# Optimization experiments

Hardware: AMD Instinct MI355X
Metric: run time of the kernel (lower is better)

The kernel has to match this reference:

```python
import jax, jax.numpy as jnp
import numpy as np
import math

N_HEADS = 8
D_EMBED = 512
D_CROSS = 768
FF_DIM = 2048
D_HEAD = D_EMBED // N_HEADS


def _gelu_tanh(x):
    # matches the module's hand-written tanh GELU
    return 0.5 * x * (1.0 + jnp.tanh(jnp.sqrt(2.0 / jnp.pi) * (x + 0.044715 * x ** 3)))


def _layer_norm(x, g, b, eps=1e-5):
    mu = jnp.mean(x, axis=-1, keepdims=True)
    var = jnp.var(x, axis=-1, keepdims=True)
    return (x - mu) * jax.lax.rsqrt(var + eps) * g + b


def setup_inputs() -> dict:
    key = jax.random.key(0)
    ks = jax.random.split(key, 20)
    s = 0.02
    inp = {
        "x": jax.random.normal(ks[0], (2, 4096, D_EMBED), jnp.float32),
        "y": jax.random.normal(ks[1], (2, 77, D_CROSS), jnp.float32),
        # self-attention: fused in_proj [D, 3D]
        "sa_in_w": jax.random.normal(ks[2], (D_EMBED, 3 * D_EMBED), jnp.float32) * s,
        "sa_in_b": jnp.zeros((3 * D_EMBED,), jnp.float32),
        "sa_out_w": jax.random.normal(ks[3], (D_EMBED, D_EMBED), jnp.float32) * s,
        "sa_out_b": jnp.zeros((D_EMBED,), jnp.float32),
        # cross-attention
        "ca_q_w": jax.random.normal(ks[4], (D_EMBED, D_EMBED), jnp.float32) * s,
        "ca_q_b": jnp.zeros((D_EMBED,), jnp.float32),
        "ca_k_w": jax.random.normal(ks[5], (D_CROSS, D_EMBED), jnp.float32) * s,
        "ca_k_b": jnp.zeros((D_EMBED,), jnp.float32),
        "ca_v_w": jax.random.normal(ks[6], (D_CROSS, D_EMBED), jnp.float32) * s,
        "ca_v_b": jnp.zeros((D_EMBED,), jnp.float32),
        "ca_out_w": jax.random.normal(ks[7], (D_EMBED, D_EMBED), jnp.float32) * s,
        "ca_out_b": jnp.zeros((D_EMBED,), jnp.float32),
        # feed-forward
        "ff_w1": jax.random.normal(ks[8], (D_EMBED, FF_DIM), jnp.float32) * s,
        "ff_b1": jnp.zeros((FF_DIM,), jnp.float32),
        "ff_w2": jax.random.normal(ks[9], (FF_DIM, D_EMBED), jnp.float32) * s,
        "ff_b2": jnp.zeros((D_EMBED,), jnp.float32),
        # layer norms
        "ln1_g": jnp.ones((D_EMBED,), jnp.float32),
        "ln1_b": jnp.zeros((D_EMBED,), jnp.float32),
        "ln2_g": jnp.ones((D_EMBED,), jnp.float32),
        "ln2_b": jnp.zeros((D_EMBED,), jnp.float32),
        "ln3_g": jnp.ones((D_EMBED,), jnp.float32),
        "ln3_b": jnp.zeros((D_EMBED,), jnp.float32),
    }
    return inp


def _mha(q, k, v):
    # q,k,v: [B, S, D] -> split heads -> attention -> merge
    B, Sq, D = q.shape
    Skv = k.shape[1]
    qh = q.reshape(B, Sq, N_HEADS, D_HEAD).transpose(0, 2, 1, 3)
    kh = k.reshape(B, Skv, N_HEADS, D_HEAD).transpose(0, 2, 1, 3)
    vh = v.reshape(B, Skv, N_HEADS, D_HEAD).transpose(0, 2, 1, 3)
    scores = jnp.einsum("bhqd,bhkd->bhqk", qh, kh) / math.sqrt(D_HEAD)
    w = jax.nn.softmax(scores, axis=-1)
    out = jnp.einsum("bhqk,bhkd->bhqd", w, vh)
    return out.transpose(0, 2, 1, 3).reshape(B, Sq, D)


def reference(x, y, sa_in_w, sa_in_b, sa_out_w, sa_out_b,
              ca_q_w, ca_q_b, ca_k_w, ca_k_b, ca_v_w, ca_v_b, ca_out_w, ca_out_b,
              ff_w1, ff_b1, ff_w2, ff_b2,
              ln1_g, ln1_b, ln2_g, ln2_b, ln3_g, ln3_b):
    # self-attention (no causal mask; default causal_mask=False)
    qkv = x @ sa_in_w + sa_in_b
    q, k, v = jnp.split(qkv, 3, axis=-1)
    sa = _mha(q, k, v) @ sa_out_w + sa_out_b
    x = _layer_norm(x + sa, ln1_g, ln1_b)

    # cross-attention to y
    qc = x @ ca_q_w + ca_q_b
    kc = y @ ca_k_w + ca_k_b
    vc = y @ ca_v_w + ca_v_b
    ca = _mha(qc, kc, vc) @ ca_out_w + ca_out_b
    x = _layer_norm(x + ca, ln2_g, ln2_b)

    # feed-forward with tanh GELU
    ff = _gelu_tanh(x @ ff_w1 + ff_b1) @ ff_w2 + ff_b2
    x = _layer_norm(x + ff, ln3_g, ln3_b)
    return x
```

## Files before the change

kernel.cpp:

```cpp
#include <hip/hip_runtime.h>
#include <stdint.h>

typedef float floatx4 __attribute__((ext_vector_type(4)));
typedef __bf16 bf16x8 __attribute__((ext_vector_type(8)));
typedef unsigned int uintx4 __attribute__((ext_vector_type(4)));
typedef unsigned short ushort_t;

__device__ __forceinline__ float b2f(ushort_t u) {
  union { unsigned int i; float f; } x; x.i = ((unsigned int)u) << 16; return x.f;
}
__device__ __forceinline__ ushort_t f2b(float f) {
  union { float f; unsigned int i; } x; x.f = f;
  unsigned int i = x.i;
  return (ushort_t)((i + 0x7FFFu + ((i >> 16) & 1u)) >> 16);
}
__device__ __forceinline__ unsigned fbits(float f) {
  union { float f; unsigned u; } x; x.f = f; return x.u;
}
__device__ __forceinline__ unsigned pk_rne(float a, float b) {
#if __has_builtin(__builtin_amdgcn_cvt_pk_bf16_f32)
  return __builtin_bit_cast(unsigned, __builtin_amdgcn_cvt_pk_bf16_f32(a, b));
#else
  return (unsigned)f2b(a) | ((unsigned)f2b(b) << 16);
#endif
}
__device__ __forceinline__ unsigned pk_fast(float a, float b) {
#if __has_builtin(__builtin_amdgcn_cvt_pk_bf16_f32)
  return __builtin_bit_cast(unsigned, __builtin_amdgcn_cvt_pk_bf16_f32(a, b));
#else
  return (fbits(b) & 0xFFFF0000u) | (fbits(a) >> 16);
#endif
}
__device__ __forceinline__ uintx4 ld16(const void* p) {
  uintx4 v; __builtin_memcpy(&v, p, 16); return v;
}
__device__ __forceinline__ void st16(void* p, uintx4 v) { __builtin_memcpy(p, &v, 16); }
__device__ __forceinline__ floatx4 f4splat(float x) { floatx4 v = {x, x, x, x}; return v; }
__device__ __forceinline__ void sched_fence() { asm volatile("" ::: "memory"); }

__device__ __forceinline__ floatx4 mfma16(uintx4 a, uintx4 b, floatx4 c) {
  return __builtin_amdgcn_mfma_f32_16x16x32_bf16(
      __builtin_bit_cast(bf16x8, a), __builtin_bit_cast(bf16x8, b), c, 0, 0, 0);
}

__device__ __forceinline__ void gll16(const ushort_t* g, ushort_t* l) {
  __builtin_amdgcn_global_load_lds(
      (__attribute__((address_space(1))) void*)(g),
      (__attribute__((address_space(3))) void*)(l), 16, 0, 0);
}

template <int EPI, int NT>
__global__ __launch_bounds__(256, 2) void gemm_bt(
    const ushort_t* __restrict__ A, const ushort_t* __restrict__ Bt,
    const float* __restrict__ bias, ushort_t* __restrict__ Cout,
    int N, int K) {
  constexpr int NI = NT / 32;
  __shared__ alignas(16) ushort_t lA[128 * 32];
  __shared__ alignas(16) ushort_t lB[NT * 32];
  const int tid = threadIdx.x;
  const int wave = tid >> 6, lane = tid & 63;
  const int quad = lane >> 4, l16 = lane & 15;
  const int bm = blockIdx.y * 128, bn = blockIdx.x * NT;
  const int wm = (wave >> 1) * 64, wn = (wave & 1) * (NT / 2);

  const ushort_t* ag0 = A + (size_t)(bm + wave * 32 + (lane >> 2)) * K + (lane & 3) * 8;
  const ushort_t* ag1 = ag0 + (size_t)16 * K;
  ushort_t* la = lA + wave * 1024;
  const ushort_t* bg0;
  const ushort_t* bg1 = nullptr;
  ushort_t* lb;
  if (NT == 128) {
    bg0 = Bt + (size_t)(bn + wave * 32 + (lane >> 2)) * K + (lane & 3) * 8;
    bg1 = bg0 + (size_t)16 * K;
    lb = lB + wave * 1024;
  } else {
    bg0 = Bt + (size_t)(bn + wave * 16 + (lane >> 2)) * K + (lane & 3) * 8;
    lb = lB + wave * 512;
  }

  floatx4 acc[4][NI];
#pragma unroll
  for (int i = 0; i < 4; i++)
#pragma unroll
    for (int j = 0; j < NI; j++) acc[i][j] = f4splat(0.f);

  for (int k0 = 0; k0 < K; k0 += 32) {
    __syncthreads();
    gll16(ag0 + k0, la);
    gll16(ag1 + k0, la + 512);
    gll16(bg0 + k0, lb);
    if (NT == 128) gll16(bg1 + k0, lb + 512);
    __syncthreads();
    uintx4 af[4], bf[NI];
#pragma unroll
    for (int i = 0; i < 4; i++) af[i] = ld16(&lA[(wm + i * 16 + l16) * 32 + quad * 8]);
#pragma unroll
    for (int i = 0; i < NI; i++) bf[i] = ld16(&lB[(wn + i * 16 + l16) * 32 + quad * 8]);
#pragma unroll
    for (int mi = 0; mi < 4; mi++)
#pragma unroll
      for (int ni = 0; ni < NI; ni++) acc[mi][ni] = mfma16(af[mi], bf[ni], acc[mi][ni]);
  }

  float bv[NI];
#pragma unroll
  for (int ni = 0; ni < NI; ni++) bv[ni] = bias[bn + wn + ni * 16 + l16];

#pragma unroll
  for (int mi = 0; mi < 4; mi++)
#pragma unroll
    for (int ni = 0; ni < NI; ni++)
#pragma unroll
      for (int r = 0; r < 4; r++) {
        int row = bm + wm + mi * 16 + quad * 4 + r;
        int col = bn + wn + ni * 16 + l16;
        float v = acc[mi][ni][r] + bv[ni];
        if (EPI == 2) {
          float w = v + 0.044715f * v * v * v;
          float e = __builtin_amdgcn_exp2f(-2.3022084f * w);
          v = v * __builtin_amdgcn_rcpf(1.f + e);
        }
        Cout[(size_t)row * N + col] = f2b(v);
      }
}

struct TransJob { const float* in; ushort_t* out; int ldi, ldo, nbx, start; };
struct TransJobs6 { TransJob j[6]; };

__global__ __launch_bounds__(256) void prep(TransJobs6 jobs, const float* __restrict__ x,
                                            ushort_t* __restrict__ xbf) {
  __shared__ float t[32][33];
  int bid = blockIdx.x;
  if (bid >= 3584) {
    int i = ((bid - 3584) * 256 + threadIdx.x) * 4;
    float4 v; __builtin_memcpy(&v, x + i, 16);
    unsigned o[2] = {pk_rne(v.x, v.y), pk_rne(v.z, v.w)};
    __builtin_memcpy(xbf + i, o, 8);
    return;
  }
  int ji = 0;
#pragma unroll
  for (int i = 1; i < 6; i++)
    if (bid >= jobs.j[i].start) ji = i;
  TransJob J = jobs.j[ji];
  int local = bid - J.start;
  int by = local / J.nbx, bx = local - by * J.nbx;
  int r0 = by * 32, c0 = bx * 32;
  int tx = threadIdx.x & 31, ty = threadIdx.x >> 5;
#pragma unroll
  for (int i = 0; i < 4; i++)
    t[ty + 8 * i][tx] = J.in[(size_t)(r0 + ty + 8 * i) * J.ldi + c0 + tx];
  __syncthreads();
#pragma unroll
  for (int i = 0; i < 4; i++)
    J.out[(size_t)(c0 + ty + 8 * i) * J.ldo + r0 + tx] = f2b(t[tx][ty + 8 * i]);
}

__global__ __launch_bounds__(256) void mid(
    const ushort_t* __restrict__ qkv, ushort_t* __restrict__ KP,
    ushort_t* __restrict__ VP, const float* __restrict__ y,
    const float* __restrict__ wk, const float* __restrict__ bk,
    const float* __restrict__ wv, const float* __restrict__ bv,
    ushort_t* __restrict__ kc, ushort_t* __restrict__ vc) {
  __shared__ ushort_t t[64 * 72];
  int bid = blockIdx.x;
  int tid = threadIdx.x;
  if (bid < 2048) {
    int g = bid * 256 + tid;
    int lane = g & 63;
    int frag = (g >> 6) & 7;
    int kt = (g >> 9) & 63;
    int bh = g >> 15;
    int b = bh >> 3, h = bh & 7;
    int ni = frag >> 1, kf = frag & 1;
    int l16 = lane & 15, quad = lane >> 4;
    const ushort_t* src = qkv + (size_t)(b * 4096 + kt * 64 + ni * 16 + l16) * 1536 +
                          512 + h * 64 + kf * 32 + quad * 8;
    st16(KP + (size_t)g * 8, ld16(src));
  } else if (bid < 3072) {
    int local = bid - 2048;
    int bh = local >> 6, kt = local & 63;
    int b = bh >> 3, h = bh & 7;
#pragma unroll
    for (int i = 0; i < 2; i++) {
      int c = i * 256 + tid;
      int row = c >> 3, c8 = (c & 7) * 8;
      uintx4 d4 = ld16(qkv + (size_t)(b * 4096 + kt * 64 + row) * 1536 + 1024 + h * 64 + c8);
      ushort_t tmp[8];
      __builtin_memcpy(tmp, &d4, 16);
#pragma unroll
      for (int j = 0; j < 8; j++) t[(c8 + j) * 72 + row] = tmp[j];
    }
    __syncthreads();
#pragma unroll
    for (int i = 0; i < 2; i++) {
      int c = i * 256 + tid;
      int frag = c >> 6, lane = c & 63;
      int f = frag >> 2, dn = frag & 3;
      int l16 = lane & 15, quad = lane >> 4;
      uintx4 d4 = ld16(&t[(dn * 16 + l16) * 72 + f * 32 + quad * 8]);
      st16(VP + ((size_t)(bh * 64 + kt) * 8 + frag) * 512 + (size_t)lane * 8, d4);
    }
  } else {
    int sb = bid - 3072;
    const float* W; const float* B; ushort_t* O;
    if (sb >= 308) { W = wv; B = bv; O = vc; sb -= 308; }
    else           { W = wk; B = bk; O = kc; }
    int idx = sb * 256 + tid;
    if (idx >= 154 * 512) return;
    int r = idx >> 9, col = idx & 511;
    const float* ya = y + (size_t)r * 768;
    float acc = B[col];
#pragma unroll 4
    for (int k = 0; k < 768; k++) acc += ya[k] * W[(size_t)k * 512 + col];
    O[idx] = f2b(acc);
  }
}

__global__ __launch_bounds__(256, 2) void flash_self(
    const ushort_t* __restrict__ qkv, const ushort_t* __restrict__ KP,
    const ushort_t* __restrict__ VP, ushort_t* __restrict__ outp) {
  __shared__ alignas(16) ushort_t lPT[4 * 32 * 72];
  const int tid = threadIdx.x, wave = tid >> 6, lane = tid & 63;
  const int quad = lane >> 4, l16 = lane & 15;
  const int bh = blockIdx.x, b = bh >> 3, h = bh & 7;
  const int qt = blockIdx.y;

  const ushort_t* Qb = qkv + (size_t)b * 4096 * 1536 + h * 64;
  const ushort_t* KPb = KP + (size_t)bh * 64 * 4096;
  const ushort_t* VPb = VP + (size_t)bh * 64 * 4096;

  uintx4 qf[2][2];
#pragma unroll
  for (int mi = 0; mi < 2; mi++)
#pragma unroll
    for (int kf = 0; kf < 2; kf++)
      qf[mi][kf] = ld16(Qb + (size_t)(qt * 128 + wave * 32 + mi * 16 + l16) * 1536 +
                        kf * 32 + quad * 8);

  floatx4 O[2][4];
#pragma unroll
  for (int mi = 0; mi < 2; mi++)
#pragma unroll
    for (int dn = 0; dn < 4; dn++) O[mi][dn] = f4splat(0.f);
  float lsum[2] = {0.f, 0.f};
  const float c = 0.18033688f;
  ushort_t* PTw = lPT + wave * 32 * 72;

#pragma unroll 2
  for (int kt = 0; kt < 64; kt++) {
    const ushort_t* kb = KPb + kt * 4096;
    uintx4 kfr[4][2];
#pragma unroll
    for (int ni = 0; ni < 4; ni++)
#pragma unroll
      for (int kf = 0; kf < 2; kf++)
        kfr[ni][kf] = ld16(kb + ((ni * 2 + kf) * 64 + lane) * 8);

    floatx4 S[2][4];
#pragma unroll
    for (int ni = 0; ni < 4; ni++)
#pragma unroll
      for (int mi = 0; mi < 2; mi++) {
        floatx4 z = f4splat(0.f);
        z = mfma16(kfr[ni][0], qf[mi][0], z);
        z = mfma16(kfr[ni][1], qf[mi][1], z);
        S[mi][ni] = z;
      }

    const ushort_t* vbp = VPb + kt * 4096;
    uintx4 vf[2][4];
#pragma unroll
    for (int f = 0; f < 2; f++)
#pragma unroll
      for (int dn = 0; dn < 4; dn++)
        vf[f][dn] = ld16(vbp + ((f * 4 + dn) * 64 + lane) * 8);

#pragma unroll
    for (int mi = 0; mi < 2; mi++) {
      float rs = 0.f;
#pragma unroll
      for (int ni = 0; ni < 4; ni++) {
        float p0 = __builtin_amdgcn_exp2f(S[mi][ni][0] * c);
        float p1 = __builtin_amdgcn_exp2f(S[mi][ni][1] * c);
        float p2 = __builtin_amdgcn_exp2f(S[mi][ni][2] * c);
        float p3 = __builtin_amdgcn_exp2f(S[mi][ni][3] * c);
        rs += (p0 + p1) + (p2 + p3);
        unsigned dd[2] = {pk_fast(p0, p1), pk_fast(p2, p3)};
        __builtin_memcpy(&PTw[(mi * 16 + l16) * 72 + ni * 16 + quad * 4], dd, 8);
      }
      lsum[mi] += rs;
    }
    sched_fence();

#pragma unroll
    for (int f = 0; f < 2; f++) {
      uintx4 pf0 = ld16(&PTw[(0 + l16) * 72 + f * 32 + quad * 8]);
      uintx4 pf1 = ld16(&PTw[(16 + l16) * 72 + f * 32 + quad * 8]);
#pragma unroll
      for (int dn = 0; dn < 4; dn++) {
        O[0][dn] = mfma16(vf[f][dn], pf0, O[0][dn]);
        O[1][dn] = mfma16(vf[f][dn], pf1, O[1][dn]);
      }
    }
  }

#pragma unroll
  for (int mi = 0; mi < 2; mi++) {
    lsum[mi] += __shfl_xor(lsum[mi], 16);
    lsum[mi] += __shfl_xor(lsum[mi], 32);
  }

#pragma unroll
  for (int mi = 0; mi < 2; mi++) {
    float inv = 1.0f / lsum[mi];
    const size_t rowg = (size_t)b * 4096 + qt * 128 + wave * 32 + mi * 16 + l16;
#pragma unroll
    for (int dn = 0; dn < 4; dn++) {
      unsigned uu[2] = {pk_rne(O[mi][dn][0] * inv, O[mi][dn][1] * inv),
                        pk_rne(O[mi][dn][2] * inv, O[mi][dn][3] * inv)};
      __builtin_memcpy(outp + rowg * 512 + h * 64 + dn * 16 + quad * 4, uu, 8);
    }
  }
}

__global__ __launch_bounds__(256, 2) void cross_attn(
    const ushort_t* __restrict__ qc, const ushort_t* __restrict__ kc,
    const ushort_t* __restrict__ vc, ushort_t* __restrict__ outp) {
  __shared__ alignas(16) ushort_t lK[96 * 72];
  __shared__ alignas(16) ushort_t lV[64 * 104];
  __shared__ alignas(16) ushort_t lP[128 * 104];
  const int tid = threadIdx.x, wave = tid >> 6, lane = tid & 63;
  const int quad = lane >> 4, l16 = lane & 15;
  const int bh = blockIdx.y, b = bh >> 3, h = bh & 7;
  const int qt = blockIdx.x;

#pragma unroll
  for (int i = 0; i < 3; i++) {
    int ch = i * 256 + tid;
    int r = ch >> 3, c8 = ch & 7;
    uintx4 d = {0u, 0u, 0u, 0u};
    if (r < 77) d = ld16(kc + (size_t)(b * 77 + r) * 512 + h * 64 + c8 * 8);
    st16(&lK[r * 72 + c8 * 8], d);
  }
  for (int i = 0; i < 24; i++) {
    int e = i * 256 + tid;
    int dd = e / 96, s = e - dd * 96;
    ushort_t v = 0;
    if (s < 77) v = vc[(size_t)(b * 77 + s) * 512 + h * 64 + dd];
    lV[dd * 104 + s] = v;
  }
  __syncthreads();

  const int qr0 = qt * 128 + wave * 32;
  uintx4 qf[2][2];
#pragma unroll
  for (int mi = 0; mi < 2; mi++)
#pragma unroll
    for (int kf = 0; kf < 2; kf++)
      qf[mi][kf] =
          ld16(qc + (size_t)(b * 4096 + qr0 + mi * 16 + l16) * 512 + h * 64 + kf * 32 + quad * 8);

  floatx4 S[2][6];
#pragma unroll
  for (int ni = 0; ni < 6; ni++) {
    uintx4 k0 = ld16(&lK[(ni * 16 + l16) * 72 + quad * 8]);
    uintx4 k1 = ld16(&lK[(ni * 16 + l16) * 72 + 32 + quad * 8]);
#pragma unroll
    for (int mi = 0; mi < 2; mi++) {
      floatx4 z = f4splat(0.f);
      z = mfma16(qf[mi][0], k0, z);
      z = mfma16(qf[mi][1], k1, z);
      S[mi][ni] = z;
    }
  }
  const float c = 0.18033688f;
#pragma unroll
  for (int ni = 4; ni < 6; ni++)
    if (ni * 16 + l16 >= 77) {
      S[0][ni] = f4splat(-1e30f);
      S[1][ni] = f4splat(-1e30f);
    }

  floatx4 linv[2];
#pragma unroll
  for (int mi = 0; mi < 2; mi++) {
    floatx4 cm = S[mi][0];
#pragma unroll
    for (int ni = 1; ni < 6; ni++)
#pragma unroll
      for (int r = 0; r < 4; r++) cm[r] = fmaxf(cm[r], S[mi][ni][r]);
#pragma unroll
    for (int off = 1; off < 16; off <<= 1)
#pragma unroll
      for (int r = 0; r < 4; r++) cm[r] = fmaxf(cm[r], __shfl_xor(cm[r], off));
    floatx4 rs = f4splat(0.f);
#pragma unroll
    for (int ni = 0; ni < 6; ni++)
#pragma unroll
      for (int r = 0; r < 4; r++) {
        float p = __builtin_amdgcn_exp2f(S[mi][ni][r] * c - cm[r] * c);
        S[mi][ni][r] = p;
        rs[r] += p;
      }
#pragma unroll
    for (int off = 1; off < 16; off <<= 1)
#pragma unroll
      for (int r = 0; r < 4; r++) rs[r] += __shfl_xor(rs[r], off);
#pragma unroll
    for (int r = 0; r < 4; r++) linv[mi][r] = 1.0f / rs[r];
#pragma unroll
    for (int ni = 0; ni < 6; ni++)
#pragma unroll
      for (int r = 0; r < 4; r++)
        lP[(wave * 32 + mi * 16 + quad * 4 + r) * 104 + ni * 16 + l16] = f2b(S[mi][ni][r]);
  }
  sched_fence();

  floatx4 O[2][4];
#pragma unroll
  for (int mi = 0; mi < 2; mi++)
#pragma unroll
    for (int dn = 0; dn < 4; dn++) O[mi][dn] = f4splat(0.f);
#pragma unroll
  for (int kf = 0; kf < 3; kf++) {
    uintx4 pa0 = ld16(&lP[(wave * 32 + 0 + l16) * 104 + kf * 32 + quad * 8]);
    uintx4 pa1 = ld16(&lP[(wave * 32 + 16 + l16) * 104 + kf * 32 + quad * 8]);
#pragma unroll
    for (int dn = 0; dn < 4; dn++) {
      uintx4 vb = ld16(&lV[(dn * 16 + l16) * 104 + kf * 32 + quad * 8]);
      O[0][dn] = mfma16(pa0, vb, O[0][dn]);
      O[1][dn] = mfma16(pa1, vb, O[1][dn]);
    }
  }
#pragma unroll
  for (int mi = 0; mi < 2; mi++)
#pragma unroll
    for (int dn = 0; dn < 4; dn++)
#pragma unroll
      for (int r = 0; r < 4; r++) {
        int row = b * 4096 + qt * 128 + wave * 32 + mi * 16 + quad * 4 + r;
        int col = h * 64 + dn * 16 + l16;
        outp[(size_t)row * 512 + col] = f2b(O[mi][dn][r] * linv[mi][r]);
      }
}

template <int RESF>
__global__ __launch_bounds__(256) void ln_kernel(
    const ushort_t* __restrict__ p, const void* __restrict__ resv,
    const float* __restrict__ g, const float* __restrict__ bb,
    float* __restrict__ out32, ushort_t* __restrict__ outbf) {
  const int row = blockIdx.x * 4 + (threadIdx.x >> 6);
  const int lane = threadIdx.x & 63;
  const size_t base = (size_t)row * 512;
  float v[8];
  float s = 0.f, ss = 0.f;
#pragma unroll
  for (int i = 0; i < 2; i++) {
    int cidx = i * 256 + lane * 4;
    ushort_t pb[4];
    __builtin_memcpy(pb, p + base + cidx, 8);
    float rv[4];
    if (RESF) {
      __builtin_memcpy(rv, (const float*)resv + base + cidx, 16);
    } else {
      ushort_t rr[4];
      __builtin_memcpy(rr, (const ushort_t*)resv + base + cidx, 8);
#pragma unroll
      for (int j = 0; j < 4; j++) rv[j] = b2f(rr[j]);
    }
#pragma unroll
    for (int j = 0; j < 4; j++) {
      float a = b2f(pb[j]) + rv[j];
      v[i * 4 + j] = a;
      s += a;
      ss += a * a;
    }
  }
#pragma unroll
  for (int off = 1; off < 64; off <<= 1) {
    s += __shfl_xor(s, off);
    ss += __shfl_xor(ss, off);
  }
  float mean = s * (1.f / 512.f);
  float var = ss * (1.f / 512.f) - mean * mean;
  float rstd = rsqrtf(var + 1e-5f);
#pragma unroll
  for (int i = 0; i < 2; i++) {
    int cidx = i * 256 + lane * 4;
    float gv[4], bv2[4];
    __builtin_memcpy(gv, g + cidx, 16);
    __builtin_memcpy(bv2, bb + cidx, 16);
    float y[4];
#pragma unroll
    for (int j = 0; j < 4; j++) y[j] = (v[i * 4 + j] - mean) * rstd * gv[j] + bv2[j];
    if (out32) __builtin_memcpy(out32 + base + cidx, y, 16);
    if (outbf) {
      unsigned o[2] = {pk_rne(y[0], y[1]), pk_rne(y[2], y[3])};
      __builtin_memcpy(outbf + base + cidx, o, 8);
    }
  }
}

extern "C" void kernel_launch(void* const* d_in, const int* in_sizes, int n_in,
                              void* d_out, int out_size, void* d_ws, size_t ws_size,
                              hipStream_t stream) {
  const size_t MiB = 1048576;
  if (ws_size < 64 * MiB) return;

  const float* x        = (const float*)d_in[0];
  const float* y        = (const float*)d_in[1];
  const float* sa_in_w  = (const float*)d_in[2];
  const float* sa_in_b  = (const float*)d_in[3];
  const float* sa_out_w = (const float*)d_in[4];
  const float* sa_out_b = (const float*)d_in[5];
  const float* ca_q_w   = (const float*)d_in[6];
  const float* ca_q_b   = (const float*)d_in[7];
  const float* ca_k_w   = (const float*)d_in[8];
  const float* ca_k_b   = (const float*)d_in[9];
  const float* ca_v_w   = (const float*)d_in[10];
  const float* ca_v_b   = (const float*)d_in[11];
  const float* ca_out_w = (const float*)d_in[12];
  const float* ca_out_b = (const float*)d_in[13];
  const float* ff_w1    = (const float*)d_in[14];
  const float* ff_b1    = (const float*)d_in[15];
  const float* ff_w2    = (const float*)d_in[16];
  const float* ff_b2    = (const float*)d_in[17];
  const float* ln1_g    = (const float*)d_in[18];
  const float* ln1_b    = (const float*)d_in[19];
  const float* ln2_g    = (const float*)d_in[20];
  const float* ln2_b    = (const float*)d_in[21];
  const float* ln3_g    = (const float*)d_in[22];
  const float* ln3_b    = (const float*)d_in[23];

  char* w = (char*)d_ws;
  ushort_t* QKV  = (ushort_t*)(w + 0);
  ushort_t* QC   = (ushort_t*)(w + 0);
  ushort_t* FF   = (ushort_t*)(w + 0);
  ushort_t* ATT  = (ushort_t*)(w + 24 * MiB);
  ushort_t* XBF  = (ushort_t*)(w + 32 * MiB);
  ushort_t* KP   = (ushort_t*)(w + 32 * MiB);
  ushort_t* XB0b = (ushort_t*)(w + 32 * MiB);
  ushort_t* VP   = (ushort_t*)(w + 40 * MiB);
  ushort_t* XB1b = (ushort_t*)(w + 40 * MiB);
  ushort_t* P    = (ushort_t*)(w + 48 * MiB);
  ushort_t* WT   = (ushort_t*)(w + 56 * MiB);
  ushort_t* KC   = (ushort_t*)(w + 63 * MiB);
  ushort_t* VC   = KC + 154 * 512;

  ushort_t* WT_sain  = WT;
  ushort_t* WT_saout = WT_sain + 786432;
  ushort_t* WT_caq   = WT_saout + 262144;
  ushort_t* WT_caout = WT_caq + 262144;
  ushort_t* WT_ff1   = WT_caout + 262144;
  ushort_t* WT_ff2   = WT_ff1 + 1048576;

  TransJobs6 tj;
  tj.j[0] = TransJob{sa_in_w,  WT_sain,  1536, 512, 48, 0};
  tj.j[1] = TransJob{sa_out_w, WT_saout, 512,  512, 16, 768};
  tj.j[2] = TransJob{ca_q_w,   WT_caq,   512,  512, 16, 1024};
  tj.j[3] = TransJob{ca_out_w, WT_caout, 512,  512, 16, 1280};
  tj.j[4] = TransJob{ff_w1,    WT_ff1,   2048, 512, 64, 1536};
  tj.j[5] = TransJob{ff_w2,    WT_ff2,   512, 2048, 16, 2560};
  prep<<<7680, 256, 0, stream>>>(tj, x, XBF);

  gemm_bt<0, 128><<<dim3(12, 64), 256, 0, stream>>>(XBF, WT_sain, sa_in_b, QKV, 1536, 512);
  mid<<<3688, 256, 0, stream>>>(QKV, KP, VP, y, ca_k_w, ca_k_b, ca_v_w, ca_v_b, KC, VC);
  flash_self<<<dim3(16, 32), 256, 0, stream>>>(QKV, KP, VP, ATT);
  gemm_bt<0, 64><<<dim3(8, 64), 256, 0, stream>>>(ATT, WT_saout, sa_out_b, P, 512, 512);
  ln_kernel<1><<<2048, 256, 0, stream>>>(P, x, ln1_g, ln1_b, nullptr, XB0b);

  gemm_bt<0, 64><<<dim3(8, 64), 256, 0, stream>>>(XB0b, WT_caq, ca_q_b, QC, 512, 512);
  cross_attn<<<dim3(32, 16), 256, 0, stream>>>(QC, KC, VC, ATT);
  gemm_bt<0, 64><<<dim3(8, 64), 256, 0, stream>>>(ATT, WT_caout, ca_out_b, P, 512, 512);
  ln_kernel<0><<<2048, 256, 0, stream>>>(P, XB0b, ln2_g, ln2_b, nullptr, XB1b);

  gemm_bt<2, 128><<<dim3(16, 64), 256, 0, stream>>>(XB1b, WT_ff1, ff_b1, FF, 2048, 512);
  gemm_bt<0, 64><<<dim3(8, 64), 256, 0, stream>>>(FF, WT_ff2, ff_b2, P, 512, 2048);
  ln_kernel<0><<<2048, 256, 0, stream>>>(P, XB1b, ln3_g, ln3_b, (float*)d_out, nullptr);
}
```

Baseline: 425.5 us.

## Compute cross-attention K/V projections with bf16 MFMA GEMMs instead of scalar loop

Replaces the naive per-element fp32 dot-product loop for the cross-attention K and V projections with two small bf16 tiled GEMM launches. The prep kernel now also transposes the K/V weights and converts y to zero-padded bf16, and the old mid kernel is reduced to a pure K/V packing kernel. This removes strided scalar weight reads from the critical path, at the cost of two extra tiny launches, extra prep blocks, and bf16 rounding of y and the weights.

```diff
diff --git a/kernel.cpp b/kernel.cpp
--- a/kernel.cpp
+++ b/kernel.cpp
@@ -125,14 +125,30 @@
 }
 
 struct TransJob { const float* in; ushort_t* out; int ldi, ldo, nbx, start; };
-struct TransJobs6 { TransJob j[6]; };
-
-__global__ __launch_bounds__(256) void prep(TransJobs6 jobs, const float* __restrict__ x,
-                                            ushort_t* __restrict__ xbf) {
+struct TransJobs8 { TransJob j[8]; };
+
+__global__ __launch_bounds__(256) void prep(TransJobs8 jobs, const float* __restrict__ x,
+                                            ushort_t* __restrict__ xbf,
+                                            const float* __restrict__ y,
+                                            ushort_t* __restrict__ ybf) {
   __shared__ float t[32][33];
   int bid = blockIdx.x;
-  if (bid >= 3584) {
-    int i = ((bid - 3584) * 256 + threadIdx.x) * 4;
+  if (bid >= 8448) {
+    int i = ((bid - 8448) * 256 + threadIdx.x) * 4;
+    const int limit = 154 * 768;
+    float v4[4];
+    if (i + 4 <= limit) {
+      __builtin_memcpy(v4, y + i, 16);
+    } else {
+#pragma unroll
+      for (int j = 0; j < 4; j++) v4[j] = (i + j < limit) ? y[i + j] : 0.f;
+    }
+    unsigned o[2] = {pk_rne(v4[0], v4[1]), pk_rne(v4[2], v4[3])};
+    __builtin_memcpy(ybf + i, o, 8);
+    return;
+  }
+  if (bid >= 4352) {
+    int i = ((bid - 4352) * 256 + threadIdx.x) * 4;
     float4 v; __builtin_memcpy(&v, x + i, 16);
     unsigned o[2] = {pk_rne(v.x, v.y), pk_rne(v.z, v.w)};
     __builtin_memcpy(xbf + i, o, 8);
@@ -140,7 +156,7 @@
   }
   int ji = 0;
 #pragma unroll
-  for (int i = 1; i < 6; i++)
+  for (int i = 1; i < 8; i++)
     if (bid >= jobs.j[i].start) ji = i;
   TransJob J = jobs.j[ji];
   int local = bid - J.start;
@@ -156,12 +172,9 @@
     J.out[(size_t)(c0 + ty + 8 * i) * J.ldo + r0 + tx] = f2b(t[tx][ty + 8 * i]);
 }
 
-__global__ __launch_bounds__(256) void mid(
+__global__ __launch_bounds__(256) void pack(
     const ushort_t* __restrict__ qkv, ushort_t* __restrict__ KP,
-    ushort_t* __restrict__ VP, const float* __restrict__ y,
-    const float* __restrict__ wk, const float* __restrict__ bk,
-    const float* __restrict__ wv, const float* __restrict__ bv,
-    ushort_t* __restrict__ kc, ushort_t* __restrict__ vc) {
+    ushort_t* __restrict__ VP) {
   __shared__ ushort_t t[64 * 72];
   int bid = blockIdx.x;
   int tid = threadIdx.x;
@@ -177,7 +190,7 @@
     const ushort_t* src = qkv + (size_t)(b * 4096 + kt * 64 + ni * 16 + l16) * 1536 +
                           512 + h * 64 + kf * 32 + quad * 8;
     st16(KP + (size_t)g * 8, ld16(src));
-  } else if (bid < 3072) {
+  } else {
     int local = bid - 2048;
     int bh = local >> 6, kt = local & 63;
     int b = bh >> 3, h = bh & 7;
@@ -201,19 +214,6 @@
       uintx4 d4 = ld16(&t[(dn * 16 + l16) * 72 + f * 32 + quad * 8]);
       st16(VP + ((size_t)(bh * 64 + kt) * 8 + frag) * 512 + (size_t)lane * 8, d4);
     }
-  } else {
-    int sb = bid - 3072;
-    const float* W; const float* B; ushort_t* O;
-    if (sb >= 308) { W = wv; B = bv; O = vc; sb -= 308; }
-    else           { W = wk; B = bk; O = kc; }
-    int idx = sb * 256 + tid;
-    if (idx >= 154 * 512) return;
-    int r = idx >> 9, col = idx & 511;
-    const float* ya = y + (size_t)r * 768;
-    float acc = B[col];
-#pragma unroll 4
-    for (int k = 0; k < 768; k++) acc += ya[k] * W[(size_t)k * 512 + col];
-    O[idx] = f2b(acc);
   }
 }
 
@@ -537,6 +537,9 @@
   ushort_t* QKV  = (ushort_t*)(w + 0);
   ushort_t* QC   = (ushort_t*)(w + 0);
   ushort_t* FF   = (ushort_t*)(w + 0);
+  ushort_t* YBF  = (ushort_t*)(w + 24 * MiB);
+  ushort_t* WTk  = (ushort_t*)(w + 24 * MiB + 524288);
+  ushort_t* WTv  = (ushort_t*)(w + 24 * MiB + 1572864);
   ushort_t* ATT  = (ushort_t*)(w + 24 * MiB);
   ushort_t* XBF  = (ushort_t*)(w + 32 * MiB);
   ushort_t* KP   = (ushort_t*)(w + 32 * MiB);
@@ -546,7 +549,7 @@
   ushort_t* P    = (ushort_t*)(w + 48 * MiB);
   ushort_t* WT   = (ushort_t*)(w + 56 * MiB);
   ushort_t* KC   = (ushort_t*)(w + 63 * MiB);
-  ushort_t* VC   = KC + 154 * 512;
+  ushort_t* VC   = KC + 256 * 512;
 
   ushort_t* WT_sain  = WT;
   ushort_t* WT_saout = WT_sain + 786432;
@@ -555,17 +558,22 @@
   ushort_t* WT_ff1   = WT_caout + 262144;
   ushort_t* WT_ff2   = WT_ff1 + 1048576;
 
-  TransJobs6 tj;
+  TransJobs8 tj;
   tj.j[0] = TransJob{sa_in_w,  WT_sain,  1536, 512, 48, 0};
   tj.j[1] = TransJob{sa_out_w, WT_saout, 512,  512, 16, 768};
   tj.j[2] = TransJob{ca_q_w,   WT_caq,   512,  512, 16, 1024};
   tj.j[3] = TransJob{ca_out_w, WT_caout, 512,  512, 16, 1280};
   tj.j[4] = TransJob{ff_w1,    WT_ff1,   2048, 512, 64, 1536};
   tj.j[5] = TransJob{ff_w2,    WT_ff2,   512, 2048, 16, 2560};
-  prep<<<7680, 256, 0, stream>>>(tj, x, XBF);
+  tj.j[6] = TransJob{ca_k_w,   WTk,      512,  768, 16, 3584};
+  tj.j[7] = TransJob{ca_v_w,   WTv,      512,  768, 16, 3968};
+  prep<<<8640, 256, 0, stream>>>(tj, x, XBF, y, YBF);
+
+  gemm_bt<0, 64><<<dim3(8, 2), 256, 0, stream>>>(YBF, WTk, ca_k_b, KC, 512, 768);
+  gemm_bt<0, 64><<<dim3(8, 2), 256, 0, stream>>>(YBF, WTv, ca_v_b, VC, 512, 768);
 
   gemm_bt<0, 128><<<dim3(12, 64), 256, 0, stream>>>(XBF, WT_sain, sa_in_b, QKV, 1536, 512);
-  mid<<<3688, 256, 0, stream>>>(QKV, KP, VP, y, ca_k_w, ca_k_b, ca_v_w, ca_v_b, KC, VC);
+  pack<<<3072, 256, 0, stream>>>(QKV, KP, VP);
   flash_self<<<dim3(16, 32), 256, 0, stream>>>(QKV, KP, VP, ATT);
   gemm_bt<0, 64><<<dim3(8, 64), 256, 0, stream>>>(ATT, WT_saout, sa_out_b, P, 512, 512);
   ln_kernel<1><<<2048, 256, 0, stream>>>(P, x, ln1_g, ln1_b, nullptr, XB0b);
```

Result: faster. 396.9 us (-6.7%).
